# Optimization experiments

Measured on AMD Instinct MI355X. Metric: run time of the kernel, lower is better.

Reference implementation:

```python
import jax, jax.numpy as jnp
import numpy as np

D = 256      # in_out_dimension
HID = 128    # hidden_dimension
N = 8192     # total nodes
S = 256      # number of graphs/segments


def setup_inputs() -> dict:
    key = jax.random.key(0)
    ks = jax.random.split(key, 20)
    lin = lambda k, o, i: jax.random.normal(k, (o, i), jnp.float32) * 0.05
    vec = lambda k, o: jax.random.normal(k, (o,), jnp.float32) * 0.05
    H = jax.random.normal(ks[0], (N, D), jnp.float32)
    batch = jnp.sort(jax.random.randint(ks[1], (N,), 0, S)).astype(jnp.int64)
    return {
        "H": H, "batch": batch,
        "phi_w1": lin(ks[2], D, D), "phi_b1": vec(ks[3], D),
        "phi_w2": lin(ks[4], D, D), "phi_b2": vec(ks[5], D),
        "att_w": lin(ks[6], D, D), "att_b": vec(ks[7], D),
        "rho_w1": lin(ks[8], D, D), "rho_b1": vec(ks[9], D),
        "rho_w2": lin(ks[10], D, D), "rho_b2": vec(ks[11], D),
        "g_w1": lin(ks[12], HID, D), "g_b1": vec(ks[13], HID),
        "g_w2": lin(ks[14], HID, HID), "g_b2": vec(ks[15], HID),
        "g_w3": lin(ks[16], 1, HID), "g_b3": vec(ks[17], 1),
    }


def _lrelu(x):
    return jax.nn.leaky_relu(x, negative_slope=0.01)


def reference(H, batch, phi_w1, phi_b1, phi_w2, phi_b2, att_w, att_b,
              rho_w1, rho_b1, rho_w2, rho_b2,
              g_w1, g_b1, g_w2, g_b2, g_w3, g_b3):
    # phi MLP
    Hf = _lrelu(_lrelu(H @ phi_w1.T + phi_b1) @ phi_w2.T + phi_b2)  # [N, D]
    att = Hf @ att_w.T + att_b                                      # [N, D]
    dot = att @ att.T                                               # [N, N]
    mask = (batch[:, None] == batch[None, :]).astype(Hf.dtype)      # block-diagonal
    # faithful to torch: max over (dot * mask), i.e. includes masked zeros
    max_values = jnp.max(dot * mask, axis=1, keepdims=True)         # [N, 1]
    mdp = (dot - max_values) * mask
    e = jnp.exp(mdp)
    aw = (e / jnp.sum(e * mask, axis=1, keepdims=True)) * mask      # [N, N]
    H_mixed = aw @ Hf                                               # [N, D]
    H_mixed = _lrelu(_lrelu(H_mixed @ rho_w1.T + rho_b1) @ rho_w2.T + rho_b2)
    h_gate = _lrelu(_lrelu(H_mixed @ g_w1.T + g_b1) @ g_w2.T + g_b2) @ g_w3.T + g_b3  # [N, 1]
    # scatter_softmax over segments
    seg_max = jax.ops.segment_max(h_gate, batch, num_segments=S)    # [S, 1]
    ex = jnp.exp(h_gate - seg_max[batch])
    den = jax.ops.segment_sum(ex, batch, num_segments=S)
    scores = ex / den[batch]                                        # [N, 1]
    h_pool = jax.ops.segment_sum(H_mixed * scores, batch, num_segments=S)  # [S, D]
    return (h_pool, scores)
```

## Files before the change

### kernel.cpp

```cpp
#include <hip/hip_runtime.h>
#include <math.h>

#define N_NODES 8192
#define D 256
#define HID 128
#define S_SEG 256
#define MAXC 64
#define HFT_STR 144
#define PB_STR 144
#define PB_LO 9216

typedef __attribute__((ext_vector_type(8))) short short8;
typedef __attribute__((ext_vector_type(4))) float f32x4;
typedef unsigned short u16;
typedef unsigned int u32;

__device__ __forceinline__ u16 f2bf(float f) {
  u32 u = __float_as_uint(f);
  u32 r = (u + 0x7fffu + ((u >> 16) & 1u)) >> 16;
  return (u16)r;
}
__device__ __forceinline__ float bf2f(u16 b) {
  return __uint_as_float(((u32)b) << 16);
}
__device__ __forceinline__ int4 pack8(float4 x, float4 y) {
  int4 v;
  v.x = (int)(((u32)f2bf(x.y) << 16) | f2bf(x.x));
  v.y = (int)(((u32)f2bf(x.w) << 16) | f2bf(x.z));
  v.z = (int)(((u32)f2bf(y.y) << 16) | f2bf(y.x));
  v.w = (int)(((u32)f2bf(y.w) << 16) | f2bf(y.z));
  return v;
}

struct CvtJobs {
  const float* src[7];
  u16* dst[7];
  int n4[7];
};
__global__ __launch_bounds__(256) void prep(const int* __restrict__ batch,
                                            int* __restrict__ sstart,
                                            int* __restrict__ scount, CvtJobs jb) {
  if (blockIdx.x == 0) {
    __shared__ int cntS[S_SEG];
    __shared__ int startS[S_SEG];
    const int t = threadIdx.x;
    cntS[t] = 0;
    startS[t] = 0;
    __syncthreads();
    const int base = t * 32;
    int pb = (base == 0) ? -1 : batch[base - 1];
    for (int i = 0; i < 32; ++i) {
      int b = batch[base + i];
      atomicAdd(&cntS[b], 1);
      if (b != pb) startS[b] = base + i;
      pb = b;
    }
    __syncthreads();
    scount[t] = cntS[t];
    sstart[t] = startS[t];
  } else {
    const int bid = blockIdx.x - 1;
    const int job = bid >> 3, chunk = bid & 7;
    const float* s = jb.src[job];
    u16* d = jb.dst[job];
    const int n4 = jb.n4[job];
    for (int i = chunk * 256 + threadIdx.x; i < n4; i += 2048) {
      float4 v = ((const float4*)s)[i];
      ushort4 o;
      o.x = f2bf(v.x); o.y = f2bf(v.y); o.z = f2bf(v.z); o.w = f2bf(v.w);
      ((ushort4*)d)[i] = o;
    }
  }
}

template <int KST>
__device__ __forceinline__ void loadW(short8* w, const u16* __restrict__ Wg,
                                      int col, int K, int lane) {
  const u16* base = Wg + (size_t)col * K + ((lane >> 4) * 8);
#pragma unroll
  for (int kk = 0; kk < KST; ++kk) w[kk] = *(const short8*)(base + kk * 32);
}

template <int KST, int ACT, int ISTR, int OSTR, int MODE, int MG>
__device__ __forceinline__ void mlp_phase(
    const u16* ldsIn, u16* ldsOut, u16* ldsOut2, const short8* wreg,
    const float* __restrict__ bias, int cg, int rows, int lane, int wave) {
  const int nrt = (rows + 31) >> 5;
  const int col = cg * 16 + (lane & 15);
  const float b = bias[col];
  int rt0, rt1;
  if constexpr (MG == 16) {
    rt0 = 0; rt1 = nrt;
  } else {
    rt0 = wave >> 3;
    rt1 = (rt0 < nrt) ? rt0 + 1 : rt0;
  }
  for (int rt = rt0; rt < rt1; ++rt) {
    short8 af[2][KST];
#pragma unroll
    for (int m = 0; m < 2; ++m)
#pragma unroll
      for (int kk = 0; kk < KST; ++kk) {
        const int r = rt * 32 + m * 16 + (lane & 15);
        const int sl = kk * 4 + (lane >> 4);
        af[m][kk] = *(const short8*)((const char*)ldsIn + r * ISTR +
                                     ((sl ^ (r & 7)) * 16));
      }
    f32x4 acc0 = {0.f, 0.f, 0.f, 0.f}, acc1 = {0.f, 0.f, 0.f, 0.f};
    __builtin_amdgcn_s_setprio(1);
#pragma unroll
    for (int kk = 0; kk < KST; ++kk) {
      acc0 = __builtin_amdgcn_mfma_f32_16x16x32_bf16(af[0][kk], wreg[kk], acc0, 0, 0, 0);
      acc1 = __builtin_amdgcn_mfma_f32_16x16x32_bf16(af[1][kk], wreg[kk], acc1, 0, 0, 0);
    }
    __builtin_amdgcn_s_setprio(0);
    const int rb = (lane >> 4) * 4;
#pragma unroll
    for (int m = 0; m < 2; ++m) {
      f32x4 a = m ? acc1 : acc0;
#pragma unroll
      for (int r4 = 0; r4 < 4; ++r4) {
        const int row = rt * 32 + m * 16 + rb + r4;
        if (row < rows) {
          float v = a[r4] + b;
          if (ACT) v = (v >= 0.f) ? v : 0.01f * v;
          if constexpr (MODE == 3) {
            const int byo =
                row * OSTR + (((col >> 3) ^ (row & 7)) * 16) + (col & 7) * 2;
            u16 hi = f2bf(v);
            *(u16*)((char*)ldsOut + byo) = hi;
            *(u16*)((char*)ldsOut2 + byo) = f2bf(v - bf2f(hi));
          } else if constexpr (MODE == 4) {
            u16 hv = f2bf(v);
            *(u16*)((char*)ldsOut + row * OSTR +
                    (((col >> 3) ^ (row & 7)) * 16) + (col & 7) * 2) = hv;
            *(u16*)((char*)ldsOut2 + col * HFT_STR + row * 2) = hv;
          } else {
            *(u16*)((char*)ldsOut + row * OSTR +
                    (((col >> 3) ^ (row & 7)) * 16) + (col & 7) * 2) = f2bf(v);
          }
        }
      }
    }
  }
}

template <int KST, int ACT, int ISTR, int OSTR, int MODE>
__device__ __forceinline__ void mlp16(
    const u16* ldsIn, u16* ldsOut, u16* ldsOut2, const u16* __restrict__ Wg,
    const float* __restrict__ bias, u16* __restrict__ gOut,
    u16* __restrict__ gOut2, int M, int K, int rows, int lane, int wave) {
  const int MG = M >> 4;
  const int npairs = ((rows + 31) >> 5) * MG;
  for (int p = wave; p < npairs; p += 16) {
    const int rt = p / MG, cg = p - rt * MG;
    short8 af[2][KST];
#pragma unroll
    for (int m = 0; m < 2; ++m)
#pragma unroll
      for (int kk = 0; kk < KST; ++kk) {
        const int r = rt * 32 + m * 16 + (lane & 15);
        const int sl = kk * 4 + (lane >> 4);
        af[m][kk] = *(const short8*)((const char*)ldsIn + r * ISTR +
                                     ((sl ^ (r & 7)) * 16));
      }
    const int col = cg * 16 + (lane & 15);
    short8 bfr[KST];
#pragma unroll
    for (int kk = 0; kk < KST; ++kk)
      bfr[kk] = *(const short8*)&Wg[(size_t)col * K + kk * 32 + (lane >> 4) * 8];
    f32x4 acc0 = {0.f, 0.f, 0.f, 0.f}, acc1 = {0.f, 0.f, 0.f, 0.f};
#pragma unroll
    for (int kk = 0; kk < KST; ++kk) {
      acc0 = __builtin_amdgcn_mfma_f32_16x16x32_bf16(af[0][kk], bfr[kk], acc0, 0, 0, 0);
      acc1 = __builtin_amdgcn_mfma_f32_16x16x32_bf16(af[1][kk], bfr[kk], acc1, 0, 0, 0);
    }
    const float b = bias[col];
    const int rb = (lane >> 4) * 4;
#pragma unroll
    for (int m = 0; m < 2; ++m) {
      f32x4 a = m ? acc1 : acc0;
#pragma unroll
      for (int r4 = 0; r4 < 4; ++r4) {
        const int row = rt * 32 + m * 16 + rb + r4;
        if (row < rows) {
          float v = a[r4] + b;
          if (ACT) v = (v >= 0.f) ? v : 0.01f * v;
          if constexpr (MODE == 2) {
            u16 hi = f2bf(v);
            gOut[(size_t)row * M + col] = hi;
            gOut2[(size_t)row * M + col] = f2bf(v - bf2f(hi));
          } else {
            u16 hv = f2bf(v);
            *(u16*)((char*)ldsOut + row * OSTR + (((col >> 3) ^ (row & 7)) * 16) +
                    (col & 7) * 2) = hv;
            if constexpr (MODE == 1) gOut[(size_t)row * M + col] = hv;
          }
        }
      }
    }
  }
}

__global__ __launch_bounds__(1024) void seg_all(
    const float* __restrict__ H, const u16* __restrict__ pw1,
    const float* __restrict__ pb1, const u16* __restrict__ pw2,
    const float* __restrict__ pb2, const u16* __restrict__ aw,
    const float* __restrict__ ab, const u16* __restrict__ rw1,
    const float* __restrict__ rb1, const u16* __restrict__ rw2,
    const float* __restrict__ rb2, const u16* __restrict__ gw1,
    const float* __restrict__ gb1, const u16* __restrict__ gw2,
    const float* __restrict__ gb2, const float* __restrict__ gw3,
    const float* __restrict__ gb3, const int* __restrict__ sstart,
    const int* __restrict__ scount, float* __restrict__ hpool,
    float* __restrict__ scores, u16* __restrict__ Hfg, u16* __restrict__ aHg,
    u16* __restrict__ aLg, u16* __restrict__ Hmg, u16* __restrict__ Hm2g,
    float* __restrict__ hgg) {
  __shared__ __align__(16) u16 bufX[MAXC * 256];
  __shared__ __align__(16) u16 bufY[MAXC * 256];
  __shared__ __align__(16) u16 attH[MAXC * 256];
  __shared__ __align__(16) u16 Tt[256 * 72];
  __shared__ float hgs[MAXC];
  __shared__ float red[1024];
  __shared__ float part[1024];
  const int s = blockIdx.x, t = threadIdx.x;
  const int cnt = scount[s];
  const int r0 = sstart[s];
  const int wave = t >> 6, lane = t & 63;

  if (cnt == 0) {
    if (t < 256) hpool[(size_t)s * D + t] = 0.f;
    return;
  }

  if (cnt <= MAXC) {
    short8 wreg[8];
    const int cg16 = (wave + s) & 15;
    const int cg8 = ((wave & 7) + s) & 7;
    const int col16 = cg16 * 16 + (lane & 15);
    const int col8 = cg8 * 16 + (lane & 15);
    const int l15 = lane & 15;

    loadW<8>(wreg, pw1, col16, D, lane);
    {
      const int r = t >> 4, p16 = t & 15;
      if (r < cnt) {
        const float4* src = (const float4*)&H[(size_t)(r0 + r) * D + p16 * 16];
#pragma unroll
        for (int i = 0; i < 2; ++i) {
          int4 v = pack8(src[2 * i], src[2 * i + 1]);
          const int sl = p16 * 2 + i;
          *(int4*)((char*)bufX + r * 512 + ((sl ^ (r & 7)) * 16)) = v;
        }
      }
    }
    __syncthreads();
    mlp_phase<8, 1, 512, 512, 0, 16>(bufX, bufY, nullptr, wreg, pb1, cg16, cnt, lane, wave);
    loadW<8>(wreg, pw2, col16, D, lane);
    __syncthreads();
    mlp_phase<8, 1, 512, 512, 4, 16>(bufY, bufX, (u16*)Tt, wreg, pb2, cg16, cnt, lane, wave);
    loadW<8>(wreg, aw, col16, D, lane);
    __syncthreads();
    mlp_phase<8, 0, 512, 512, 3, 16>(bufX, attH, bufY, wreg, ab, cg16, cnt, lane, wave);
    loadW<8>(wreg, rw1, col16, D, lane);
    __syncthreads();
    const int cp = (cnt + 15) & ~15;
    const int nt = cp >> 4;
    const int cpk = (cp <= 32) ? 32 : 64;
    if (wave < nt) {
      const int ti = wave;
      const int ra = ti * 16 + l15;
      f32x4 evt[4];
      f32x4 rs = {0.f, 0.f, 0.f, 0.f};
#pragma unroll
      for (int tj = 0; tj < 4; ++tj) {
        if (tj < nt) {
          const int rj = tj * 16 + l15;
          f32x4 acc = {0.f, 0.f, 0.f, 0.f};
          __builtin_amdgcn_s_setprio(1);
#pragma unroll
          for (int k0 = 0; k0 < D; k0 += 32) {
            const int sg = (k0 >> 3) + (lane >> 4);
            short8 ah = *(const short8*)((const char*)attH + ra * 512 + ((sg ^ (ra & 7)) * 16));
            short8 av = *(const short8*)((const char*)bufY + ra * 512 + ((sg ^ (ra & 7)) * 16));
            short8 bh = *(const short8*)((const char*)attH + rj * 512 + ((sg ^ (rj & 7)) * 16));
            short8 bv = *(const short8*)((const char*)bufY + rj * 512 + ((sg ^ (rj & 7)) * 16));
            acc = __builtin_amdgcn_mfma_f32_16x16x32_bf16(ah, bh, acc, 0, 0, 0);
            acc = __builtin_amdgcn_mfma_f32_16x16x32_bf16(ah, bv, acc, 0, 0, 0);
            acc = __builtin_amdgcn_mfma_f32_16x16x32_bf16(av, bh, acc, 0, 0, 0);
          }
          __builtin_amdgcn_s_setprio(0);
          const bool jok = (tj * 16 + l15) < cnt;
          f32x4 ev;
#pragma unroll
          for (int r = 0; r < 4; ++r) ev[r] = jok ? __expf(acc[r]) : 0.f;
          evt[tj] = ev;
          float p0 = ev[0], p1 = ev[1], p2 = ev[2], p3 = ev[3];
#pragma unroll
          for (int o = 1; o <= 8; o <<= 1) {
            p0 += __shfl_xor(p0, o); p1 += __shfl_xor(p1, o);
            p2 += __shfl_xor(p2, o); p3 += __shfl_xor(p3, o);
          }
          rs[0] += p0; rs[1] += p1; rs[2] += p2; rs[3] += p3;
        }
      }
      const int rbase = ti * 16 + (lane >> 4) * 4;
#pragma unroll
      for (int tj = 0; tj < 4; ++tj) {
        if (tj < nt) {
          const int j = tj * 16 + l15;
#pragma unroll
          for (int r = 0; r < 4; ++r) {
            const float pv = evt[tj][r] / rs[r];
            const u16 hi = f2bf(pv);
            *(u16*)((char*)bufX + (rbase + r) * PB_STR + j * 2) = hi;
            *(u16*)((char*)bufX + PB_LO + (rbase + r) * PB_STR + j * 2) =
                f2bf(pv - bf2f(hi));
          }
        }
      }
    }
    if (cpk > cp) {
      for (int idx = t; idx < cp * 16; idx += 1024) {
        const int rr = idx >> 4, cc = cp + (idx & 15);
        *(u16*)((char*)bufX + rr * PB_STR + cc * 2) = 0;
        *(u16*)((char*)bufX + PB_LO + rr * PB_STR + cc * 2) = 0;
      }
    }
    if (cpk > cnt) {
      const int w3 = cpk - cnt;
      for (int idx = t; idx < 256 * w3; idx += 1024) {
        const int dd = idx / w3, cc = cnt + idx - (idx / w3) * w3;
        *(u16*)((char*)Tt + dd * HFT_STR + cc * 2) = 0;
      }
    }
    __syncthreads();
    {
      const int kst = cpk >> 5;
      for (int tt = wave; tt < nt * 16; tt += 16) {
        const int rt = tt >> 4, cg = tt & 15;
        const int arow = rt * 16 + l15;
        const int dcol = cg * 16 + l15;
        const int koct = (lane >> 4) * 8;
        f32x4 acc = {0.f, 0.f, 0.f, 0.f};
        __builtin_amdgcn_s_setprio(1);
        for (int ks = 0; ks < kst; ++ks) {
          const int kb = ks * 32 + koct;
          short8 ph = *(const short8*)((const char*)bufX + arow * PB_STR + kb * 2);
          short8 pl = *(const short8*)((const char*)bufX + PB_LO + arow * PB_STR + kb * 2);
          short8 hb = *(const short8*)((const char*)Tt + dcol * HFT_STR + kb * 2);
          acc = __builtin_amdgcn_mfma_f32_16x16x32_bf16(ph, hb, acc, 0, 0, 0);
          acc = __builtin_amdgcn_mfma_f32_16x16x32_bf16(pl, hb, acc, 0, 0, 0);
        }
        __builtin_amdgcn_s_setprio(0);
        const int rb = (lane >> 4) * 4;
#pragma unroll
        for (int r = 0; r < 4; ++r) {
          const int row = rt * 16 + rb + r;
          const int col = cg * 16 + l15;
          *(u16*)((char*)attH + row * 512 + (((col >> 3) ^ (row & 7)) * 16) +
                  (col & 7) * 2) = f2bf(acc[r]);
        }
      }
    }
    __syncthreads();
    mlp_phase<8, 1, 512, 512, 0, 16>(attH, bufY, nullptr, wreg, rb1, cg16, cnt, lane, wave);
    loadW<8>(wreg, rw2, col16, D, lane);
    __syncthreads();
    mlp_phase<8, 1, 512, 512, 0, 16>(bufY, (u16*)Tt, nullptr, wreg, rb2, cg16, cnt, lane, wave);
    loadW<8>(wreg, gw1, col8, D, lane);
    __syncthreads();
    if (t < 64) hgs[t] = 0.f;
    mlp_phase<8, 1, 512, 256, 0, 8>((u16*)Tt, bufX, nullptr, wreg, gb1, cg8, cnt, lane, wave);
    loadW<4>(wreg, gw2, col8, HID, lane);
    __syncthreads();
    {
      const int nrt = (cnt + 31) >> 5;
      const int rt = wave >> 3;
      if (rt < nrt) {
        short8 af2[2][4];
#pragma unroll
        for (int m = 0; m < 2; ++m)
#pragma unroll
          for (int kk = 0; kk < 4; ++kk) {
            const int r = rt * 32 + m * 16 + l15;
            const int sl = kk * 4 + (lane >> 4);
            af2[m][kk] = *(const short8*)((const char*)bufX + r * 256 +
                                          ((sl ^ (r & 7)) * 16));
          }
        f32x4 acc0 = {0.f, 0.f, 0.f, 0.f}, acc1 = {0.f, 0.f, 0.f, 0.f};
        __builtin_amdgcn_s_setprio(1);
#pragma unroll
        for (int kk = 0; kk < 4; ++kk) {
          acc0 = __builtin_amdgcn_mfma_f32_16x16x32_bf16(af2[0][kk], wreg[kk], acc0, 0, 0, 0);
          acc1 = __builtin_amdgcn_mfma_f32_16x16x32_bf16(af2[1][kk], wreg[kk], acc1, 0, 0, 0);
        }
        __builtin_amdgcn_s_setprio(0);
        const float b = gb2[col8];
        const float w3c = gw3[col8];
        const int rb = (lane >> 4) * 4;
#pragma unroll
        for (int m = 0; m < 2; ++m) {
          f32x4 a = m ? acc1 : acc0;
#pragma unroll
          for (int r4 = 0; r4 < 4; ++r4) {
            const int row = rt * 32 + m * 16 + rb + r4;
            float v = a[r4] + b;
            v = (v >= 0.f) ? v : 0.01f * v;
            float pp = v * w3c;
            pp += __shfl_xor(pp, 1);
            pp += __shfl_xor(pp, 2);
            pp += __shfl_xor(pp, 4);
            pp += __shfl_xor(pp, 8);
            if ((lane & 15) == 0 && row < cnt) atomicAdd(&hgs[row], pp);
          }
        }
      }
    }
    __syncthreads();
    {
      const float hgv = (lane < cnt) ? hgs[lane] : -INFINITY;
      float m = hgv;
#pragma unroll
      for (int o = 32; o > 0; o >>= 1) m = fmaxf(m, __shfl_xor(m, o));
      float e = (lane < cnt) ? __expf(hgv - m) : 0.f;
      float sum = e;
#pragma unroll
      for (int o = 32; o > 0; o >>= 1) sum += __shfl_xor(sum, o);
      const float sc = e / sum;
      if (wave == 0 && lane < cnt) scores[r0 + lane] = sc;
      const int d = (wave & 3) * 64 + lane;
      const int g = wave >> 2;
      float acc = 0.f;
      for (int i = g; i < cnt; i += 4) {
        const float si = __shfl(sc, i);
        acc += si * bf2f(*(const u16*)((const char*)Tt + i * 512 +
                          (((d >> 3) ^ (i & 7)) * 16) + (d & 7) * 2));
      }
      part[g * 256 + d] = acc;
    }
    __syncthreads();
    if (t < 256)
      hpool[(size_t)s * D + t] =
          part[t] + part[t + 256] + part[t + 512] + part[t + 768];
  } else {
    for (int c0 = 0; c0 < cnt; c0 += 64) {
      const int rows = (cnt - c0) > 64 ? 64 : (cnt - c0);
      {
        const int r = t >> 4, p16 = t & 15;
        if (r < rows) {
          const float4* src = (const float4*)&H[(size_t)(r0 + c0 + r) * D + p16 * 16];
#pragma unroll
          for (int i = 0; i < 2; ++i) {
            int4 v = pack8(src[2 * i], src[2 * i + 1]);
            const int sl = p16 * 2 + i;
            *(int4*)((char*)bufX + r * 512 + ((sl ^ (r & 7)) * 16)) = v;
          }
        }
      }
      __syncthreads();
      mlp16<8, 1, 512, 512, 0>(bufX, bufY, nullptr, pw1, pb1, nullptr, nullptr, D, D, rows, lane, wave);
      __syncthreads();
      mlp16<8, 1, 512, 512, 1>(bufY, bufX, nullptr, pw2, pb2, Hfg + (size_t)(r0 + c0) * D, nullptr, D, D, rows, lane, wave);
      __syncthreads();
      mlp16<8, 0, 512, 512, 2>(bufX, nullptr, nullptr, aw, ab, aHg + (size_t)(r0 + c0) * D, aLg + (size_t)(r0 + c0) * D, D, D, rows, lane, wave);
      __syncthreads();
    }
    float* Pf = (float*)bufY;
    for (int i = 0; i < cnt; ++i) {
      const u16* ai = aHg + (size_t)(r0 + i) * D;
      const u16* li = aLg + (size_t)(r0 + i) * D;
      for (int j = t; j < cnt; j += 1024) {
        const u16* aj = aHg + (size_t)(r0 + j) * D;
        const u16* lj = aLg + (size_t)(r0 + j) * D;
        float acc = 0.f;
        for (int k = 0; k < D; ++k)
          acc += (bf2f(ai[k]) + bf2f(li[k])) * (bf2f(aj[k]) + bf2f(lj[k]));
        Pf[j] = acc;
      }
      __syncthreads();
      float pm = -INFINITY;
      for (int j = t; j < cnt; j += 1024) pm = fmaxf(pm, Pf[j]);
      red[t] = pm;
      __syncthreads();
      for (int o = 512; o > 0; o >>= 1) {
        if (t < o) red[t] = fmaxf(red[t], red[t + o]);
        __syncthreads();
      }
      const float m = red[0];
      __syncthreads();
      float ps = 0.f;
      for (int j = t; j < cnt; j += 1024) {
        const float e = __expf(Pf[j] - m);
        Pf[j] = e;
        ps += e;
      }
      red[t] = ps;
      __syncthreads();
      for (int o = 512; o > 0; o >>= 1) {
        if (t < o) red[t] += red[t + o];
        __syncthreads();
      }
      const float inv = 1.f / red[0];
      if (t < D) {
        float acc = 0.f;
        for (int j = 0; j < cnt; ++j)
          acc += Pf[j] * bf2f(Hfg[(size_t)(r0 + j) * D + t]);
        Hmg[(size_t)(r0 + i) * D + t] = f2bf(acc * inv);
      }
      __syncthreads();
    }
    for (int c0 = 0; c0 < cnt; c0 += 64) {
      const int rows = (cnt - c0) > 64 ? 64 : (cnt - c0);
      {
        const int r = t >> 4, p16 = t & 15;
        if (r < rows) {
          const int4* src = (const int4*)&Hmg[(size_t)(r0 + c0 + r) * D + p16 * 16];
#pragma unroll
          for (int i = 0; i < 2; ++i) {
            const int sl = p16 * 2 + i;
            *(int4*)((char*)bufX + r * 512 + ((sl ^ (r & 7)) * 16)) = src[i];
          }
        }
      }
      __syncthreads();
      mlp16<8, 1, 512, 512, 0>(bufX, bufY, nullptr, rw1, rb1, nullptr, nullptr, D, D, rows, lane, wave);
      __syncthreads();
      mlp16<8, 1, 512, 512, 1>(bufY, bufX, nullptr, rw2, rb2, Hm2g + (size_t)(r0 + c0) * D, nullptr, D, D, rows, lane, wave);
      __syncthreads();
      mlp16<8, 1, 512, 256, 0>(bufX, bufY, nullptr, gw1, gb1, nullptr, nullptr, HID, D, rows, lane, wave);
      __syncthreads();
      mlp16<4, 1, 256, 256, 0>(bufY, attH, nullptr, gw2, gb2, nullptr, nullptr, HID, HID, rows, lane, wave);
      __syncthreads();
      {
        const int i = t >> 4, p16 = t & 15;
        if (i < rows) {
          short8 hv = *(const short8*)((const char*)attH + i * 256 + ((p16 ^ (i & 7)) * 16));
          float sacc = 0.f;
#pragma unroll
          for (int q = 0; q < 8; ++q) sacc += bf2f((u16)hv[q]) * gw3[p16 * 8 + q];
          sacc += __shfl_xor(sacc, 1);
          sacc += __shfl_xor(sacc, 2);
          sacc += __shfl_xor(sacc, 4);
          sacc += __shfl_xor(sacc, 8);
          if (p16 == 0) hgg[r0 + c0 + i] = sacc + gb3[0];
        }
      }
      __syncthreads();
    }
    float pm = -INFINITY;
    for (int i = t; i < cnt; i += 1024) pm = fmaxf(pm, hgg[r0 + i]);
    red[t] = pm;
    __syncthreads();
    for (int o = 512; o > 0; o >>= 1) {
      if (t < o) red[t] = fmaxf(red[t], red[t + o]);
      __syncthreads();
    }
    const float m = red[0];
    __syncthreads();
    float ps = 0.f;
    for (int i = t; i < cnt; i += 1024) ps += __expf(hgg[r0 + i] - m);
    red[t] = ps;
    __syncthreads();
    for (int o = 512; o > 0; o >>= 1) {
      if (t < o) red[t] += red[t + o];
      __syncthreads();
    }
    const float inv = 1.f / red[0];
    for (int i = t; i < cnt; i += 1024)
      scores[r0 + i] = __expf(hgg[r0 + i] - m) * inv;
    const int h = t >> 8, d = t & 255;
    float acc = 0.f;
    for (int i = h; i < cnt; i += 4)
      acc += __expf(hgg[r0 + i] - m) * inv * bf2f(Hm2g[(size_t)(r0 + i) * D + d]);
    part[t] = acc;
    __syncthreads();
    if (t < 256)
      hpool[(size_t)s * D + t] =
          part[t] + part[t + 256] + part[t + 512] + part[t + 768];
  }
}

extern "C" void kernel_launch(void* const* d_in, const int* in_sizes, int n_in,
                              void* d_out, int out_size, void* d_ws, size_t ws_size,
                              hipStream_t stream) {
  const float* H      = (const float*)d_in[0];
  const int*   batch  = (const int*)d_in[1];
  const float* phi_w1 = (const float*)d_in[2];
  const float* phi_b1 = (const float*)d_in[3];
  const float* phi_w2 = (const float*)d_in[4];
  const float* phi_b2 = (const float*)d_in[5];
  const float* att_w  = (const float*)d_in[6];
  const float* att_b  = (const float*)d_in[7];
  const float* rho_w1 = (const float*)d_in[8];
  const float* rho_b1 = (const float*)d_in[9];
  const float* rho_w2 = (const float*)d_in[10];
  const float* rho_b2 = (const float*)d_in[11];
  const float* g_w1   = (const float*)d_in[12];
  const float* g_b1   = (const float*)d_in[13];
  const float* g_w2   = (const float*)d_in[14];
  const float* g_b2   = (const float*)d_in[15];
  const float* g_w3   = (const float*)d_in[16];
  const float* g_b3   = (const float*)d_in[17];

  float* out_hpool  = (float*)d_out;
  float* out_scores = (float*)d_out + (size_t)S_SEG * D;

  char* w = (char*)d_ws;
  const size_t MB = 1u << 20;
  u16*   wb     = (u16*)(w);
  u16*   Hfg    = (u16*)(w + 1 * MB);
  u16*   aHg    = (u16*)(w + 5 * MB);
  u16*   aLg    = (u16*)(w + 9 * MB);
  u16*   Hmg    = (u16*)(w + 13 * MB);
  u16*   Hm2g   = (u16*)(w + 17 * MB);
  float* hgg    = (float*)(w + 21 * MB);
  int*   sstart = (int*)(w + 21 * MB + 64 * 1024);
  int*   scount = sstart + S_SEG;

  u16* phi_w1b = wb;
  u16* phi_w2b = wb + 65536;
  u16* att_wb  = wb + 2 * 65536;
  u16* rho_w1b = wb + 3 * 65536;
  u16* rho_w2b = wb + 4 * 65536;
  u16* g_w1b   = wb + 5 * 65536;
  u16* g_w2b   = wb + 5 * 65536 + 32768;

  CvtJobs jb;
  jb.src[0] = phi_w1; jb.dst[0] = phi_w1b; jb.n4[0] = 65536 / 4;
  jb.src[1] = phi_w2; jb.dst[1] = phi_w2b; jb.n4[1] = 65536 / 4;
  jb.src[2] = att_w;  jb.dst[2] = att_wb;  jb.n4[2] = 65536 / 4;
  jb.src[3] = rho_w1; jb.dst[3] = rho_w1b; jb.n4[3] = 65536 / 4;
  jb.src[4] = rho_w2; jb.dst[4] = rho_w2b; jb.n4[4] = 65536 / 4;
  jb.src[5] = g_w1;   jb.dst[5] = g_w1b;   jb.n4[5] = 32768 / 4;
  jb.src[6] = g_w2;   jb.dst[6] = g_w2b;   jb.n4[6] = 16384 / 4;

  prep<<<57, 256, 0, stream>>>(batch, sstart, scount, jb);

  seg_all<<<S_SEG, 1024, 0, stream>>>(
      H, phi_w1b, phi_b1, phi_w2b, phi_b2, att_wb, att_b, rho_w1b, rho_b1,
      rho_w2b, rho_b2, g_w1b, g_b1, g_w2b, g_b2, g_w3, g_b3, sstart, scount,
      out_hpool, out_scores, Hfg, aHg, aLg, Hmg, Hm2g, hgg);
}
```

Baseline: 53.28 us.

## Use 32x32x16 MFMA on eight waves for the 256-wide MLP layers

Replaces the 16x16x32 MFMA per-layer matmuls, run on 16 waves, with a 32x32x16 MFMA variant run on 8 waves, each computing a 32-column slab over up to 64 rows. Weights are split into two K halves: the first half is prefetched into registers before the barrier and the second half is loaded inside the phase. This cuts per-output LDS A-fragment reads and overlaps weight loads with the barrier wait. In exchange, half the waves sit idle during these layers and register pressure goes up from the 16-wide accumulators and the two weight buffers.

Result: faster. 49.59 us (-6.9%).

```diff
diff --git a/kernel.cpp b/kernel.cpp
--- a/kernel.cpp
+++ b/kernel.cpp
@@ -12,6 +12,7 @@
 
 typedef __attribute__((ext_vector_type(8))) short short8;
 typedef __attribute__((ext_vector_type(4))) float f32x4;
+typedef __attribute__((ext_vector_type(16))) float f32x16;
 typedef unsigned short u16;
 typedef unsigned int u32;
 
@@ -81,9 +82,87 @@
   for (int kk = 0; kk < KST; ++kk) w[kk] = *(const short8*)(base + kk * 32);
 }
 
-template <int KST, int ACT, int ISTR, int OSTR, int MODE, int MG>
+__device__ __forceinline__ void loadWh(short8* w, const u16* __restrict__ Wg,
+                                       int col, int half, int kh) {
+  const u16* base = Wg + (size_t)col * 256 + half * 128 + kh * 8;
+#pragma unroll
+  for (int kk = 0; kk < 8; ++kk) w[kk] = *(const short8*)(base + kk * 16);
+}
+
+template <int ACT, int MODE>
+__device__ __forceinline__ void mlp32(
+    const u16* ldsIn, u16* ldsOut, u16* ldsOut2, short8* wpre, short8* wcur,
+    const u16* __restrict__ Wg, const float* __restrict__ bias, int cp,
+    int rows, int lane) {
+  const int l31 = lane & 31;
+  const int kh = lane >> 5;
+  const int col = cp * 32 + l31;
+  loadWh(wcur, Wg, col, 1, kh);
+  const float b = bias[col];
+  const int nrt = (rows + 31) >> 5;
+  const int r0r = l31, r1r = 32 + l31;
+  f32x16 acc0, acc1;
+#pragma unroll
+  for (int i = 0; i < 16; ++i) { acc0[i] = 0.f; acc1[i] = 0.f; }
+  __builtin_amdgcn_s_setprio(1);
+#pragma unroll
+  for (int kk = 0; kk < 8; ++kk) {
+    const int slot = kk * 2 + kh;
+    short8 a0 = *(const short8*)((const char*)ldsIn + r0r * 512 +
+                                 ((slot ^ (r0r & 7)) * 16));
+    acc0 = __builtin_amdgcn_mfma_f32_32x32x16_bf16(a0, wpre[kk], acc0, 0, 0, 0);
+    if (nrt > 1) {
+      short8 a1 = *(const short8*)((const char*)ldsIn + r1r * 512 +
+                                   ((slot ^ (r1r & 7)) * 16));
+      acc1 = __builtin_amdgcn_mfma_f32_32x32x16_bf16(a1, wpre[kk], acc1, 0, 0, 0);
+    }
+  }
+#pragma unroll
+  for (int kk = 0; kk < 8; ++kk) {
+    const int slot = (8 + kk) * 2 + kh;
+    short8 a0 = *(const short8*)((const char*)ldsIn + r0r * 512 +
+                                 ((slot ^ (r0r & 7)) * 16));
+    acc0 = __builtin_amdgcn_mfma_f32_32x32x16_bf16(a0, wcur[kk], acc0, 0, 0, 0);
+    if (nrt > 1) {
+      short8 a1 = *(const short8*)((const char*)ldsIn + r1r * 512 +
+                                   ((slot ^ (r1r & 7)) * 16));
+      acc1 = __builtin_amdgcn_mfma_f32_32x32x16_bf16(a1, wcur[kk], acc1, 0, 0, 0);
+    }
+  }
+  __builtin_amdgcn_s_setprio(0);
+#pragma unroll
+  for (int rt = 0; rt < 2; ++rt) {
+    if (rt == 1 && nrt < 2) break;
+    const f32x16 A = rt ? acc1 : acc0;
+#pragma unroll
+    for (int reg = 0; reg < 16; ++reg) {
+      const int row = rt * 32 + (reg & 3) + 8 * (reg >> 2) + 4 * kh;
+      if (row < rows) {
+        float v = A[reg] + b;
+        if (ACT) v = (v >= 0.f) ? v : 0.01f * v;
+        if constexpr (MODE == 3) {
+          const int byo =
+              row * 512 + (((col >> 3) ^ (row & 7)) * 16) + (col & 7) * 2;
+          u16 hi = f2bf(v);
+          *(u16*)((char*)ldsOut + byo) = hi;
+          *(u16*)((char*)ldsOut2 + byo) = f2bf(v - bf2f(hi));
+        } else if constexpr (MODE == 4) {
+          u16 hv = f2bf(v);
+          *(u16*)((char*)ldsOut + row * 512 + (((col >> 3) ^ (row & 7)) * 16) +
+                  (col & 7) * 2) = hv;
+          *(u16*)((char*)ldsOut2 + col * HFT_STR + row * 2) = hv;
+        } else {
+          *(u16*)((char*)ldsOut + row * 512 + (((col >> 3) ^ (row & 7)) * 16) +
+                  (col & 7) * 2) = f2bf(v);
+        }
+      }
+    }
+  }
+}
+
+template <int KST, int ACT, int ISTR, int OSTR, int MG>
 __device__ __forceinline__ void mlp_phase(
-    const u16* ldsIn, u16* ldsOut, u16* ldsOut2, const short8* wreg,
+    const u16* ldsIn, u16* ldsOut, const short8* wreg,
     const float* __restrict__ bias, int cg, int rows, int lane, int wave) {
   const int nrt = (rows + 31) >> 5;
   const int col = cg * 16 + (lane & 15);
@@ -124,21 +203,8 @@
         if (row < rows) {
           float v = a[r4] + b;
           if (ACT) v = (v >= 0.f) ? v : 0.01f * v;
-          if constexpr (MODE == 3) {
-            const int byo =
-                row * OSTR + (((col >> 3) ^ (row & 7)) * 16) + (col & 7) * 2;
-            u16 hi = f2bf(v);
-            *(u16*)((char*)ldsOut + byo) = hi;
-            *(u16*)((char*)ldsOut2 + byo) = f2bf(v - bf2f(hi));
-          } else if constexpr (MODE == 4) {
-            u16 hv = f2bf(v);
-            *(u16*)((char*)ldsOut + row * OSTR +
-                    (((col >> 3) ^ (row & 7)) * 16) + (col & 7) * 2) = hv;
-            *(u16*)((char*)ldsOut2 + col * HFT_STR + row * 2) = hv;
-          } else {
-            *(u16*)((char*)ldsOut + row * OSTR +
-                    (((col >> 3) ^ (row & 7)) * 16) + (col & 7) * 2) = f2bf(v);
-          }
+          *(u16*)((char*)ldsOut + row * OSTR + (((col >> 3) ^ (row & 7)) * 16) +
+                  (col & 7) * 2) = f2bf(v);
         }
       }
     }
@@ -234,14 +300,16 @@
   }
 
   if (cnt <= MAXC) {
-    short8 wreg[8];
-    const int cg16 = (wave + s) & 15;
+    short8 wpre[8], wcur[8], wreg[8];
+    const bool w8 = wave < 8;
+    const int cp = (wave + s) & 7;
     const int cg8 = ((wave & 7) + s) & 7;
-    const int col16 = cg16 * 16 + (lane & 15);
     const int col8 = cg8 * 16 + (lane & 15);
     const int l15 = lane & 15;
-
-    loadW<8>(wreg, pw1, col16, D, lane);
+    const int l31 = lane & 31;
+    const int kh = lane >> 5;
+
+    if (w8) loadWh(wpre, pw1, cp * 32 + l31, 0, kh);
     {
       const int r = t >> 4, p16 = t & 15;
       if (r < cnt) {
@@ -255,18 +323,24 @@
       }
     }
     __syncthreads();
-    mlp_phase<8, 1, 512, 512, 0, 16>(bufX, bufY, nullptr, wreg, pb1, cg16, cnt, lane, wave);
-    loadW<8>(wreg, pw2, col16, D, lane);
-    __syncthreads();
-    mlp_phase<8, 1, 512, 512, 4, 16>(bufY, bufX, (u16*)Tt, wreg, pb2, cg16, cnt, lane, wave);
-    loadW<8>(wreg, aw, col16, D, lane);
-    __syncthreads();
-    mlp_phase<8, 0, 512, 512, 3, 16>(bufX, attH, bufY, wreg, ab, cg16, cnt, lane, wave);
-    loadW<8>(wreg, rw1, col16, D, lane);
-    __syncthreads();
-    const int cp = (cnt + 15) & ~15;
-    const int nt = cp >> 4;
-    const int cpk = (cp <= 32) ? 32 : 64;
+    if (w8) {
+      mlp32<1, 0>(bufX, bufY, nullptr, wpre, wcur, pw1, pb1, cp, cnt, lane);
+      loadWh(wpre, pw2, cp * 32 + l31, 0, kh);
+    }
+    __syncthreads();
+    if (w8) {
+      mlp32<1, 4>(bufY, bufX, (u16*)Tt, wpre, wcur, pw2, pb2, cp, cnt, lane);
+      loadWh(wpre, aw, cp * 32 + l31, 0, kh);
+    }
+    __syncthreads();
+    if (w8) {
+      mlp32<0, 3>(bufX, attH, bufY, wpre, wcur, aw, ab, cp, cnt, lane);
+      loadWh(wpre, rw1, cp * 32 + l31, 0, kh);
+    }
+    __syncthreads();
+    const int cpd = (cnt + 15) & ~15;
+    const int nt = cpd >> 4;
+    const int cpk = (cpd <= 32) ? 32 : 64;
     if (wave < nt) {
       const int ti = wave;
       const int ra = ti * 16 + l15;
@@ -320,9 +394,9 @@
         }
       }
     }
-    if (cpk > cp) {
-      for (int idx = t; idx < cp * 16; idx += 1024) {
-        const int rr = idx >> 4, cc = cp + (idx & 15);
+    if (cpk > cpd) {
+      for (int idx = t; idx < cpd * 16; idx += 1024) {
+        const int rr = idx >> 4, cc = cpd + (idx & 15);
         *(u16*)((char*)bufX + rr * PB_STR + cc * 2) = 0;
         *(u16*)((char*)bufX + PB_LO + rr * PB_STR + cc * 2) = 0;
       }
@@ -364,14 +438,17 @@
       }
     }
     __syncthreads();
-    mlp_phase<8, 1, 512, 512, 0, 16>(attH, bufY, nullptr, wreg, rb1, cg16, cnt, lane, wave);
-    loadW<8>(wreg, rw2, col16, D, lane);
-    __syncthreads();
-    mlp_phase<8, 1, 512, 512, 0, 16>(bufY, (u16*)Tt, nullptr, wreg, rb2, cg16, cnt, lane, wave);
+    if (w8) {
+      mlp32<1, 0>(attH, bufY, nullptr, wpre, wcur, rw1, rb1, cp, cnt, lane);
+      loadWh(wpre, rw2, cp * 32 + l31, 0, kh);
+    }
+    __syncthreads();
+    if (w8)
+      mlp32<1, 0>(bufY, (u16*)Tt, nullptr, wpre, wcur, rw2, rb2, cp, cnt, lane);
     loadW<8>(wreg, gw1, col8, D, lane);
     __syncthreads();
     if (t < 64) hgs[t] = 0.f;
-    mlp_phase<8, 1, 512, 256, 0, 8>((u16*)Tt, bufX, nullptr, wreg, gb1, cg8, cnt, lane, wave);
+    mlp_phase<8, 1, 512, 256, 8>((u16*)Tt, bufX, wreg, gb1, cg8, cnt, lane, wave);
     loadW<4>(wreg, gw2, col8, HID, lane);
     __syncthreads();
     {
```
